# Optimization experiments

Measured on AMD Instinct MI355X. Metric: run time of the kernel, lower is better.

The kernel has to match this reference:

```python
import jax, jax.numpy as jnp
import numpy as np

B, V_IN, V_OUT, C_IN, C_OUT, K, NNZ = 16, 1024, 4096, 128, 256, 18, 16384

def setup_inputs() -> dict:
    key = jax.random.key(0)
    ks = jax.random.split(key, 10)
    def lin(k, fan_in, fan_out):
        s = 1.0 / np.sqrt(fan_in)
        return jax.random.normal(k, (fan_in, fan_out), jnp.float32) * s
    return {
        "x": jax.random.normal(ks[0], (B, V_IN, C_IN), jnp.float32),
        "vals": jax.random.uniform(ks[1], (NNZ,), jnp.float32),
        "W1": lin(ks[2], 1 * C_IN, C_OUT),
        "b1": jnp.zeros((C_OUT,), jnp.float32),
        "Wd3": lin(ks[3], (K // 3) * C_IN, C_OUT // 4),
        "bd3": jnp.zeros((C_OUT // 4,), jnp.float32),
        "W2d3": lin(ks[4], (K // 3 * 2) * C_IN, C_OUT // 4),
        "b2d3": jnp.zeros((C_OUT // 4,), jnp.float32),
        "Wf": lin(ks[5], K * C_IN, C_OUT // 2),
        "bf": jnp.zeros((C_OUT // 2,), jnp.float32),
        "rows": jax.random.randint(ks[6], (NNZ,), 0, V_OUT, jnp.int32),
        "cols": jax.random.randint(ks[7], (NNZ,), 0, V_IN, jnp.int32),
        "spiral_idx": jax.random.randint(ks[8], (V_OUT, K), 0, V_OUT, jnp.int32),
    }

def _pool(x, rows, cols, vals, dim_size):
    # sparse upsample: gather cols, scale, scatter-add to rows
    gathered = x[:, cols, :] * vals[None, :, None]  # [B, nnz, C]
    return jnp.zeros((x.shape[0], dim_size, x.shape[2]), x.dtype).at[:, rows, :].add(gathered)

def _spiral_conv(feat, idx, W, b):
    # gather fixed spiral neighborhoods then shared linear layer
    Bz, V, C = feat.shape[0], idx.shape[0], feat.shape[2]
    g = feat[:, idx.reshape(-1), :].reshape(Bz, V, idx.shape[1] * C)  # [B, V, K*C]
    return g @ W + b

def reference(x, vals, W1, b1, Wd3, bd3, W2d3, b2d3, Wf, bf, rows, cols, spiral_idx):
    out = _pool(x, rows, cols, vals, V_OUT)  # [B, V_OUT, C_IN]
    k = spiral_idx.shape[1]
    short_cut = _spiral_conv(out, spiral_idx[:, :1], W1, b1)
    p_d3 = _spiral_conv(out, spiral_idx[:, : k // 3], Wd3, bd3)
    p_2d3 = _spiral_conv(out, spiral_idx[:, : k // 3 * 2], W2d3, b2d3)
    p = _spiral_conv(out, spiral_idx, Wf, bf)
    f = jnp.concatenate((p, p_2d3, p_d3), axis=2)  # [B, V_OUT, C_OUT]
    return jax.nn.relu(short_cut + f)
```

## Files before the change

kernel.cpp:

```cpp
#include <hip/hip_runtime.h>
#include <hip/hip_bf16.h>

#define B_SZ   16
#define V_IN   1024
#define V_OUT  4096
#define C_IN   128
#define C_OUT  256
#define K_NB   18
#define NNZ    16384
#define K_GEMM (K_NB * C_IN)
#define BK     64
#define NKT    (K_GEMM / BK)

typedef __attribute__((ext_vector_type(8))) short bf16x8;
typedef __attribute__((ext_vector_type(4))) float f32x4;

#define GLOAD16(src, dst) __builtin_amdgcn_global_load_lds( \
    (const __attribute__((address_space(1))) unsigned int*)(src), \
    (__attribute__((address_space(3))) unsigned int*)(dst), 16, 0, 0)

#define MFMA16(a_, b_, c_) __builtin_amdgcn_mfma_f32_16x16x32_bf16((a_), (b_), (c_), 0, 0, 0)

__global__ __launch_bounds__(1024) void csr_kernel(const int* __restrict__ rows,
                                                   int* __restrict__ offsets,
                                                   int* __restrict__ perm) {
    __shared__ int cnt[V_OUT];
    __shared__ int wsum[16];
    const int t = threadIdx.x;
    const int lane = t & 63, wid = t >> 6;
#pragma unroll
    for (int i = t; i < V_OUT; i += 1024) cnt[i] = 0;
    __syncthreads();
#pragma unroll
    for (int n = t; n < NNZ; n += 1024) atomicAdd(&cnt[rows[n]], 1);
    __syncthreads();
    const int base4 = t * 4;
    int c0 = cnt[base4], c1 = cnt[base4 + 1], c2 = cnt[base4 + 2], c3 = cnt[base4 + 3];
    int tot = c0 + c1 + c2 + c3;
    int v = tot;
#pragma unroll
    for (int d = 1; d < 64; d <<= 1) {
        int u = __shfl_up(v, d);
        if (lane >= d) v += u;
    }
    if (lane == 63) wsum[wid] = v;
    __syncthreads();
    int wbase = 0;
#pragma unroll
    for (int w = 0; w < 16; ++w) wbase += (w < wid) ? wsum[w] : 0;
    int incl = wbase + v;
    int excl = incl - tot;
    offsets[base4]     = excl;
    offsets[base4 + 1] = excl + c0;
    offsets[base4 + 2] = excl + c0 + c1;
    offsets[base4 + 3] = excl + c0 + c1 + c2;
    if (t == 1023) offsets[V_OUT] = incl;
    __syncthreads();
    cnt[base4]     = excl;
    cnt[base4 + 1] = excl + c0;
    cnt[base4 + 2] = excl + c0 + c1;
    cnt[base4 + 3] = excl + c0 + c1 + c2;
    __syncthreads();
#pragma unroll
    for (int n = t; n < NNZ; n += 1024) {
        int pos = atomicAdd(&cnt[rows[n]], 1);
        perm[pos] = n;
    }
}

__global__ __launch_bounds__(512) void pool_kernel(
    const float* __restrict__ x, const float* __restrict__ vals,
    const int* __restrict__ cols, const int* __restrict__ offsets,
    const int* __restrict__ perm, __hip_bfloat16* __restrict__ pool) {
    int r = blockIdx.x;
    int t = threadIdx.x;
    int b = t >> 5, c4 = t & 31;
    int j0 = offsets[r], j1 = offsets[r + 1];
    const float4* xb = (const float4*)x + (size_t)b * (V_IN * 32);
    float4 acc = {0.f, 0.f, 0.f, 0.f};
    for (int j = j0; j < j1; ++j) {
        int n = perm[j];
        float v = vals[n];
        float4 xv = xb[cols[n] * 32 + c4];
        acc.x += v * xv.x; acc.y += v * xv.y; acc.z += v * xv.z; acc.w += v * xv.w;
    }
    ushort4 o;
    o.x = __builtin_bit_cast(unsigned short, __float2bfloat16(acc.x));
    o.y = __builtin_bit_cast(unsigned short, __float2bfloat16(acc.y));
    o.z = __builtin_bit_cast(unsigned short, __float2bfloat16(acc.z));
    o.w = __builtin_bit_cast(unsigned short, __float2bfloat16(acc.w));
    ((ushort4*)pool)[((size_t)b * V_OUT + r) * 32 + c4] = o;
}

__global__ void wcomb_kernel(const float* __restrict__ W1, const float* __restrict__ Wd3,
                             const float* __restrict__ W2d3, const float* __restrict__ Wf,
                             const float* __restrict__ b1, const float* __restrict__ bd3,
                             const float* __restrict__ b2d3, const float* __restrict__ bf,
                             __hip_bfloat16* __restrict__ wTs, float* __restrict__ bias) {
    int idx = blockIdx.x * blockDim.x + threadIdx.x;
    if (idx >= NKT * 16384) {
        int c = idx - NKT * 16384;
        if (c < C_OUT) {
            float v = b1[c];
            if (c < 128)      v += bf[c];
            else if (c < 192) v += b2d3[c - 128];
            else              v += bd3[c - 192];
            bias[c] = v;
        }
        return;
    }
    int kt = idx >> 14;
    int c  = (idx >> 3) & 2047;
    int e  = idx & 7;
    int nrow  = c >> 3;
    int kslot = (c & 7) << 4;
    int kb = kslot ^ ((nrow & 7) << 4);
    int r  = kt * 64 + (kb >> 1) + e;
    int col = nrow;
    float v;
    if (col < 128)      v = Wf[r * 128 + col];
    else if (col < 192) v = (r < 1536) ? W2d3[r * 64 + (col - 128)] : 0.f;
    else                v = (r < 768)  ? Wd3[r * 64 + (col - 192)]  : 0.f;
    if (r < 128) v += W1[r * 256 + col];
    wTs[idx] = __float2bfloat16(v);
}

__global__ __launch_bounds__(1024, 4) void gemm_kernel(
    const __hip_bfloat16* __restrict__ pool,
    const __hip_bfloat16* __restrict__ wTs,
    const float* __restrict__ bias,
    const int* __restrict__ spiral,
    float* __restrict__ out)
{
    __shared__ __align__(16) char smem[116736];
    int* spl = (int*)(smem + 98304);

    const int tid  = threadIdx.x;
    const int lane = tid & 63;
    const int wid  = tid >> 6;
    const int wc   = wid & 3;
    const int wm   = (wid >> 2) << 6;

    const int bid = blockIdx.x;
    const int bm  = ((bid & 7) << 5) + (bid >> 3);
    const int b   = bm >> 4;
    const int v0  = (bm & 15) << 8;

    for (int i = tid; i < 256 * K_NB; i += 1024) spl[i] = spiral[v0 * K_NB + i];
    asm volatile("s_waitcnt vmcnt(0) lgkmcnt(0)" ::: "memory");
    __builtin_amdgcn_s_barrier();

    const char* poolBytes = (const char*)(pool + (size_t)b * V_OUT * C_IN);
    const char* wTsBytes  = (const char*)wTs;
    const int sb = ((tid & 7) << 4) ^ (((tid >> 3) & 7) << 4);

    auto stageA = [&](int kt) {
        const int j   = kt >> 1;
        const int c0b = (kt & 1) << 7;
        char* dst = smem + ((kt & 1) << 15);
#pragma unroll
        for (int ch = 0; ch < 2; ++ch) {
            int flat = (ch << 10) + tid;
            int sidx = spl[(flat >> 3) * K_NB + j];
            GLOAD16(poolBytes + ((size_t)sidx << 8) + (c0b + sb), dst + flat * 16);
        }
    };
    auto stageB = [&](int kt) {
        const char* src = wTsBytes + ((size_t)kt << 15);
        char* dst = smem + 65536 + ((kt & 1) << 14);
        int off = tid << 4;
        GLOAD16(src + off, dst + off);
    };

    const int l15   = lane & 15;
    const int swm   = (lane & 7) << 4;
    const int klane = (lane >> 4) << 4;
    const int kk0   = klane ^ swm;
    const int kk1   = (64 + klane) ^ swm;
    const int aBase = (wm + l15) << 7;
    const int bOff0 = (((2 * wc)     << 4) + l15) << 7;
    const int bOff1 = (((2 * wc + 1) << 4) + l15) << 7;
    const int bOff2 = (((8 + wc)     << 4) + l15) << 7;
    const int bOff3 = (((12 + wc)    << 4) + l15) << 7;

    f32x4 acc[4][4] = {};

    stageA(0);
    stageB(0);

    for (int kt = 0; kt < NKT; ++kt) {
        const int s = kt & 1;
        const char* As = smem + (s << 15);
        const char* Bs = smem + 65536 + (s << 14);
        const char* wKt = wTsBytes + ((size_t)kt << 15);

        if (kt + 1 < NKT) {
            stageA(kt + 1);
            asm volatile("s_waitcnt vmcnt(2)" ::: "memory");
        } else {
            asm volatile("s_waitcnt vmcnt(0)" ::: "memory");
        }
        __builtin_amdgcn_s_barrier();
        __builtin_amdgcn_sched_barrier(0);

        const bool doMid   = kt < 24;
        const bool doShort = kt < 12;

        bf16x8 g20, g21, g30, g31;
        if (doMid)   { g20 = *(const bf16x8*)(wKt + bOff2 + kk0);
                       g21 = *(const bf16x8*)(wKt + bOff2 + kk1); }
        if (doShort) { g30 = *(const bf16x8*)(wKt + bOff3 + kk0);
                       g31 = *(const bf16x8*)(wKt + bOff3 + kk1); }

        {
            bf16x8 a0 = *(const bf16x8*)(As + aBase + (0 << 11) + kk0);
            bf16x8 a1 = *(const bf16x8*)(As + aBase + (1 << 11) + kk0);
            bf16x8 a2 = *(const bf16x8*)(As + aBase + (2 << 11) + kk0);
            bf16x8 a3 = *(const bf16x8*)(As + aBase + (3 << 11) + kk0);
            bf16x8 bb0 = *(const bf16x8*)(Bs + bOff0 + kk0);
            bf16x8 bb1 = *(const bf16x8*)(Bs + bOff1 + kk0);
            __builtin_amdgcn_s_setprio(1);
            acc[0][0] = MFMA16(a0, bb0, acc[0][0]);
            acc[1][0] = MFMA16(a1, bb0, acc[1][0]);
            acc[2][0] = MFMA16(a2, bb0, acc[2][0]);
            acc[3][0] = MFMA16(a3, bb0, acc[3][0]);
            acc[0][1] = MFMA16(a0, bb1, acc[0][1]);
            acc[1][1] = MFMA16(a1, bb1, acc[1][1]);
            acc[2][1] = MFMA16(a2, bb1, acc[2][1]);
            acc[3][1] = MFMA16(a3, bb1, acc[3][1]);
            __builtin_amdgcn_s_setprio(0);
            if (doMid) {
                __builtin_amdgcn_s_setprio(1);
                acc[0][2] = MFMA16(a0, g20, acc[0][2]);
                acc[1][2] = MFMA16(a1, g20, acc[1][2]);
                acc[2][2] = MFMA16(a2, g20, acc[2][2]);
                acc[3][2] = MFMA16(a3, g20, acc[3][2]);
                __builtin_amdgcn_s_setprio(0);
            }
            if (doShort) {
                __builtin_amdgcn_s_setprio(1);
                acc[0][3] = MFMA16(a0, g30, acc[0][3]);
                acc[1][3] = MFMA16(a1, g30, acc[1][3]);
                acc[2][3] = MFMA16(a2, g30, acc[2][3]);
                acc[3][3] = MFMA16(a3, g30, acc[3][3]);
                __builtin_amdgcn_s_setprio(0);
            }
            if (kt + 1 < NKT) stageB(kt + 1);
        }

        {
            bf16x8 a0 = *(const bf16x8*)(As + aBase + (0 << 11) + kk1);
            bf16x8 a1 = *(const bf16x8*)(As + aBase + (1 << 11) + kk1);
            bf16x8 a2 = *(const bf16x8*)(As + aBase + (2 << 11) + kk1);
            bf16x8 a3 = *(const bf16x8*)(As + aBase + (3 << 11) + kk1);
            bf16x8 bb0 = *(const bf16x8*)(Bs + bOff0 + kk1);
            bf16x8 bb1 = *(const bf16x8*)(Bs + bOff1 + kk1);
            __builtin_amdgcn_s_setprio(1);
            acc[0][0] = MFMA16(a0, bb0, acc[0][0]);
            acc[1][0] = MFMA16(a1, bb0, acc[1][0]);
            acc[2][0] = MFMA16(a2, bb0, acc[2][0]);
            acc[3][0] = MFMA16(a3, bb0, acc[3][0]);
            acc[0][1] = MFMA16(a0, bb1, acc[0][1]);
            acc[1][1] = MFMA16(a1, bb1, acc[1][1]);
            acc[2][1] = MFMA16(a2, bb1, acc[2][1]);
            acc[3][1] = MFMA16(a3, bb1, acc[3][1]);
            __builtin_amdgcn_s_setprio(0);
            if (doMid) {
                __builtin_amdgcn_s_setprio(1);
                acc[0][2] = MFMA16(a0, g21, acc[0][2]);
                acc[1][2] = MFMA16(a1, g21, acc[1][2]);
                acc[2][2] = MFMA16(a2, g21, acc[2][2]);
                acc[3][2] = MFMA16(a3, g21, acc[3][2]);
                __builtin_amdgcn_s_setprio(0);
            }
            if (doShort) {
                __builtin_amdgcn_s_setprio(1);
                acc[0][3] = MFMA16(a0, g31, acc[0][3]);
                acc[1][3] = MFMA16(a1, g31, acc[1][3]);
                acc[2][3] = MFMA16(a2, g31, acc[2][3]);
                acc[3][3] = MFMA16(a3, g31, acc[3][3]);
                __builtin_amdgcn_s_setprio(0);
            }
        }

        __builtin_amdgcn_s_barrier();
        __builtin_amdgcn_sched_barrier(0);
    }

    const int nt[4] = {2 * wc, 2 * wc + 1, 8 + wc, 12 + wc};
#pragma unroll
    for (int ni = 0; ni < 4; ++ni) {
        int col = (nt[ni] << 4) + l15;
        float bz = bias[col];
#pragma unroll
        for (int mi = 0; mi < 4; ++mi) {
            int row0 = v0 + wm + mi * 16 + ((lane >> 4) << 2);
#pragma unroll
            for (int r4 = 0; r4 < 4; ++r4) {
                float v = acc[mi][ni][r4] + bz;
                out[((size_t)(b * V_OUT + row0 + r4)) * C_OUT + col] = v > 0.f ? v : 0.f;
            }
        }
    }
}

extern "C" void kernel_launch(void* const* d_in, const int* in_sizes, int n_in,
                              void* d_out, int out_size, void* d_ws, size_t ws_size,
                              hipStream_t stream) {
    const float* x     = (const float*)d_in[0];
    const float* vals  = (const float*)d_in[1];
    const float* W1    = (const float*)d_in[2];
    const float* b1    = (const float*)d_in[3];
    const float* Wd3   = (const float*)d_in[4];
    const float* bd3   = (const float*)d_in[5];
    const float* W2d3  = (const float*)d_in[6];
    const float* b2d3  = (const float*)d_in[7];
    const float* Wf    = (const float*)d_in[8];
    const float* bf    = (const float*)d_in[9];
    const int*   rows  = (const int*)d_in[10];
    const int*   cols  = (const int*)d_in[11];
    const int*   spiral= (const int*)d_in[12];
    float* out = (float*)d_out;

    char* ws = (char*)d_ws;
    __hip_bfloat16* pool = (__hip_bfloat16*)ws;
    __hip_bfloat16* wTs  = (__hip_bfloat16*)(ws + 16777216);
    float* bias          = (float*)(ws + 16777216 + 1179648);
    int*   offsets       = (int*)(ws + 16777216 + 1179648 + 1024);
    int*   perm          = offsets + V_OUT + 4;

    csr_kernel<<<1, 1024, 0, stream>>>(rows, offsets, perm);
    pool_kernel<<<V_OUT, 512, 0, stream>>>(x, vals, cols, offsets, perm, pool);
    wcomb_kernel<<<(NKT * 16384 + C_OUT + 255) / 256, 256, 0, stream>>>(
        W1, Wd3, W2d3, Wf, b1, bd3, b2d3, bf, wTs, bias);
    gemm_kernel<<<256, 1024, 0, stream>>>(pool, wTs, bias, spiral, out);
}
```

Baseline: 122.0 us.

## Stage full weight tile in LDS and coalesce weight-combine reads via LDS image

After: 128.0 us. +4.9%, slower.

```diff
diff --git a/kernel.cpp b/kernel.cpp
--- a/kernel.cpp
+++ b/kernel.cpp
@@ -92,37 +92,58 @@
     ((ushort4*)pool)[((size_t)b * V_OUT + r) * 32 + c4] = o;
 }
 
-__global__ void wcomb_kernel(const float* __restrict__ W1, const float* __restrict__ Wd3,
-                             const float* __restrict__ W2d3, const float* __restrict__ Wf,
-                             const float* __restrict__ b1, const float* __restrict__ bd3,
-                             const float* __restrict__ b2d3, const float* __restrict__ bf,
-                             __hip_bfloat16* __restrict__ wTs, float* __restrict__ bias) {
-    int idx = blockIdx.x * blockDim.x + threadIdx.x;
-    if (idx >= NKT * 16384) {
-        int c = idx - NKT * 16384;
-        if (c < C_OUT) {
-            float v = b1[c];
-            if (c < 128)      v += bf[c];
-            else if (c < 192) v += b2d3[c - 128];
-            else              v += bd3[c - 192];
-            bias[c] = v;
-        }
+__global__ __launch_bounds__(256) void wcomb_kernel(
+    const float* __restrict__ W1, const float* __restrict__ Wd3,
+    const float* __restrict__ W2d3, const float* __restrict__ Wf,
+    const float* __restrict__ b1, const float* __restrict__ bd3,
+    const float* __restrict__ b2d3, const float* __restrict__ bf,
+    __hip_bfloat16* __restrict__ wTs, float* __restrict__ bias) {
+    const int kt = blockIdx.x;
+    const int t  = threadIdx.x;
+    if (kt == NKT) {
+        float v = b1[t];
+        if (t < 128)      v += bf[t];
+        else if (t < 192) v += b2d3[t - 128];
+        else              v += bd3[t - 192];
+        bias[t] = v;
         return;
     }
-    int kt = idx >> 14;
-    int c  = (idx >> 3) & 2047;
-    int e  = idx & 7;
-    int nrow  = c >> 3;
-    int kslot = (c & 7) << 4;
-    int kb = kslot ^ ((nrow & 7) << 4);
-    int r  = kt * 64 + (kb >> 1) + e;
-    int col = nrow;
-    float v;
-    if (col < 128)      v = Wf[r * 128 + col];
-    else if (col < 192) v = (r < 1536) ? W2d3[r * 64 + (col - 128)] : 0.f;
-    else                v = (r < 768)  ? Wd3[r * 64 + (col - 192)]  : 0.f;
-    if (r < 128) v += W1[r * 256 + col];
-    wTs[idx] = __float2bfloat16(v);
+    __shared__ __hip_bfloat16 img[16384];
+    const int k0 = kt * 64;
+
+    auto put = [&](int col, int kl, float v) {
+        int kb    = (kl >> 3) << 4;
+        int kslot = kb ^ ((col & 7) << 4);
+        int idx   = (((col << 3) | (kslot >> 4)) << 3) | (kl & 7);
+        img[idx] = __float2bfloat16(v);
+    };
+
+    for (int i = t; i < 64 * 128; i += 256) {
+        int kl = i >> 7, col = i & 127;
+        int r  = k0 + kl;
+        float v = Wf[r * 128 + col];
+        if (r < 128) v += W1[r * 256 + col];
+        put(col, kl, v);
+    }
+    for (int i = t; i < 64 * 64; i += 256) {
+        int kl = i >> 6, c2 = i & 63;
+        int r  = k0 + kl, col = 128 + c2;
+        float v = (r < 1536) ? W2d3[r * 64 + c2] : 0.f;
+        if (r < 128) v += W1[r * 256 + col];
+        put(col, kl, v);
+    }
+    for (int i = t; i < 64 * 64; i += 256) {
+        int kl = i >> 6, c2 = i & 63;
+        int r  = k0 + kl, col = 192 + c2;
+        float v = (r < 768) ? Wd3[r * 64 + c2] : 0.f;
+        if (r < 128) v += W1[r * 256 + col];
+        put(col, kl, v);
+    }
+    __syncthreads();
+    ulonglong2* dst = (ulonglong2*)(wTs + (size_t)kt * 16384);
+    const ulonglong2* srcv = (const ulonglong2*)img;
+#pragma unroll
+    for (int i = t; i < 2048; i += 256) dst[i] = srcv[i];
 }
 
 __global__ __launch_bounds__(1024, 4) void gemm_kernel(
@@ -132,8 +153,8 @@
     const int* __restrict__ spiral,
     float* __restrict__ out)
 {
-    __shared__ __align__(16) char smem[116736];
-    int* spl = (int*)(smem + 98304);
+    __shared__ __align__(16) char smem[149504];
+    int* spl = (int*)(smem + 131072);
 
     const int tid  = threadIdx.x;
     const int lane = tid & 63;
@@ -167,16 +188,17 @@
     };
     auto stageB = [&](int kt) {
         const char* src = wTsBytes + ((size_t)kt << 15);
-        char* dst = smem + 65536 + ((kt & 1) << 14);
-        int off = tid << 4;
-        GLOAD16(src + off, dst + off);
+        char* dst = smem + 65536 + ((kt & 1) << 15);
+#pragma unroll
+        for (int ch = 0; ch < 2; ++ch) {
+            int off = ((ch << 10) + tid) << 4;
+            GLOAD16(src + off, dst + off);
+        }
     };
 
     const int l15   = lane & 15;
     const int swm   = (lane & 7) << 4;
     const int klane = (lane >> 4) << 4;
-    const int kk0   = klane ^ swm;
-    const int kk1   = (64 + klane) ^ swm;
     const int aBase = (wm + l15) << 7;
     const int bOff0 = (((2 * wc)     << 4) + l15) << 7;
     const int bOff1 = (((2 * wc + 1) << 4) + l15) << 7;
@@ -191,8 +213,7 @@
     for (int kt = 0; kt < NKT; ++kt) {
         const int s = kt & 1;
         const char* As = smem + (s << 15);
-        const char* Bs = smem + 65536 + (s << 14);
-        const char* wKt = wTsBytes + ((size_t)kt << 15);
+        const char* Bs = smem + 65536 + (s << 15);
 
         if (kt + 1 < NKT) {
             stageA(kt + 1);
@@ -206,19 +227,15 @@
         const bool doMid   = kt < 24;
         const bool doShort = kt < 12;
 
-        bf16x8 g20, g21, g30, g31;
-        if (doMid)   { g20 = *(const bf16x8*)(wKt + bOff2 + kk0);
-                       g21 = *(const bf16x8*)(wKt + bOff2 + kk1); }
-        if (doShort) { g30 = *(const bf16x8*)(wKt + bOff3 + kk0);
-                       g31 = *(const bf16x8*)(wKt + bOff3 + kk1); }
-
-        {
-            bf16x8 a0 = *(const bf16x8*)(As + aBase + (0 << 11) + kk0);
-            bf16x8 a1 = *(const bf16x8*)(As + aBase + (1 << 11) + kk0);
-            bf16x8 a2 = *(const bf16x8*)(As + aBase + (2 << 11) + kk0);
-            bf16x8 a3 = *(const bf16x8*)(As + aBase + (3 << 11) + kk0);
-            bf16x8 bb0 = *(const bf16x8*)(Bs + bOff0 + kk0);
-            bf16x8 bb1 = *(const bf16x8*)(Bs + bOff1 + kk0);
+#pragma unroll
+        for (int ks = 0; ks < 2; ++ks) {
+            const int kk = (ks * 64 + klane) ^ swm;
+            bf16x8 a0 = *(const bf16x8*)(As + aBase + (0 << 11) + kk);
+            bf16x8 a1 = *(const bf16x8*)(As + aBase + (1 << 11) + kk);
+            bf16x8 a2 = *(const bf16x8*)(As + aBase + (2 << 11) + kk);
+            bf16x8 a3 = *(const bf16x8*)(As + aBase + (3 << 11) + kk);
+            bf16x8 bb0 = *(const bf16x8*)(Bs + bOff0 + kk);
+            bf16x8 bb1 = *(const bf16x8*)(Bs + bOff1 + kk);
             __builtin_amdgcn_s_setprio(1);
             acc[0][0] = MFMA16(a0, bb0, acc[0][0]);
             acc[1][0] = MFMA16(a1, bb0, acc[1][0]);
@@ -230,57 +247,24 @@
             acc[3][1] = MFMA16(a3, bb1, acc[3][1]);
             __builtin_amdgcn_s_setprio(0);
             if (doMid) {
+                bf16x8 bb2 = *(const bf16x8*)(Bs + bOff2 + kk);
                 __builtin_amdgcn_s_setprio(1);
-                acc[0][2] = MFMA16(a0, g20, acc[0][2]);
-                acc[1][2] = MFMA16(a1, g20, acc[1][2]);
-                acc[2][2] = MFMA16(a2, g20, acc[2][2]);
-                acc[3][2] = MFMA16(a3, g20, acc[3][2]);
+                acc[0][2] = MFMA16(a0, bb2, acc[0][2]);
+                acc[1][2] = MFMA16(a1, bb2, acc[1][2]);
+                acc[2][2] = MFMA16(a2, bb2, acc[2][2]);
+                acc[3][2] = MFMA16(a3, bb2, acc[3][2]);
                 __builtin_amdgcn_s_setprio(0);
             }
             if (doShort) {
+                bf16x8 bb3 = *(const bf16x8*)(Bs + bOff3 + kk);
                 __builtin_amdgcn_s_setprio(1);
-                acc[0][3] = MFMA16(a0, g30, acc[0][3]);
-                acc[1][3] = MFMA16(a1, g30, acc[1][3]);
-                acc[2][3] = MFMA16(a2, g30, acc[2][3]);
-                acc[3][3] = MFMA16(a3, g30, acc[3][3]);
+                acc[0][3] = MFMA16(a0, bb3, acc[0][3]);
+                acc[1][3] = MFMA16(a1, bb3, acc[1][3]);
+                acc[2][3] = MFMA16(a2, bb3, acc[2][3]);
+                acc[3][3] = MFMA16(a3, bb3, acc[3][3]);
                 __builtin_amdgcn_s_setprio(0);
             }
-            if (kt + 1 < NKT) stageB(kt + 1);
-        }
-
-        {
-            bf16x8 a0 = *(const bf16x8*)(As + aBase + (0 << 11) + kk1);
-            bf16x8 a1 = *(const bf16x8*)(As + aBase + (1 << 11) + kk1);
-            bf16x8 a2 = *(const bf16x8*)(As + aBase + (2 << 11) + kk1);
-            bf16x8 a3 = *(const bf16x8*)(As + aBase + (3 << 11) + kk1);
-            bf16x8 bb0 = *(const bf16x8*)(Bs + bOff0 + kk1);
-            bf16x8 bb1 = *(const bf16x8*)(Bs + bOff1 + kk1);
-            __builtin_amdgcn_s_setprio(1);
-            acc[0][0] = MFMA16(a0, bb0, acc[0][0]);
-            acc[1][0] = MFMA16(a1, bb0, acc[1][0]);
-            acc[2][0] = MFMA16(a2, bb0, acc[2][0]);
-            acc[3][0] = MFMA16(a3, bb0, acc[3][0]);
-            acc[0][1] = MFMA16(a0, bb1, acc[0][1]);
-            acc[1][1] = MFMA16(a1, bb1, acc[1][1]);
-            acc[2][1] = MFMA16(a2, bb1, acc[2][1]);
-            acc[3][1] = MFMA16(a3, bb1, acc[3][1]);
-            __builtin_amdgcn_s_setprio(0);
-            if (doMid) {
-                __builtin_amdgcn_s_setprio(1);
-                acc[0][2] = MFMA16(a0, g21, acc[0][2]);
-                acc[1][2] = MFMA16(a1, g21, acc[1][2]);
-                acc[2][2] = MFMA16(a2, g21, acc[2][2]);
-                acc[3][2] = MFMA16(a3, g21, acc[3][2]);
-                __builtin_amdgcn_s_setprio(0);
-            }
-            if (doShort) {
-                __builtin_amdgcn_s_setprio(1);
-                acc[0][3] = MFMA16(a0, g31, acc[0][3]);
-                acc[1][3] = MFMA16(a1, g31, acc[1][3]);
-                acc[2][3] = MFMA16(a2, g31, acc[2][3]);
-                acc[3][3] = MFMA16(a3, g31, acc[3][3]);
-                __builtin_amdgcn_s_setprio(0);
-            }
+            if (ks == 0 && kt + 1 < NKT) stageB(kt + 1);
         }
 
         __builtin_amdgcn_s_barrier();
@@ -331,7 +315,6 @@
 
     csr_kernel<<<1, 1024, 0, stream>>>(rows, offsets, perm);
     pool_kernel<<<V_OUT, 512, 0, stream>>>(x, vals, cols, offsets, perm, pool);
-    wcomb_kernel<<<(NKT * 16384 + C_OUT + 255) / 256, 256, 0, stream>>>(
-        W1, Wd3, W2d3, Wf, b1, bd3, b2d3, bf, wTs, bias);
+    wcomb_kernel<<<NKT + 1, 256, 0, stream>>>(W1, Wd3, W2d3, Wf, b1, bd3, b2d3, bf, wTs, bias);
     gemm_kernel<<<256, 1024, 0, stream>>>(pool, wTs, bias, spiral, out);
 }
```
